# Kernel optimization log

Measured on AMD Instinct MI355X. Metric: run time of the kernel, lower is better.

The kernel has to match this reference:

```python
import jax, jax.numpy as jnp
import numpy as np


def _next_pow2(n: int) -> int:
    return 1 << (int(n) - 1).bit_length()


def setup_inputs() -> dict:
    key = jax.random.key(0)
    k1, k2 = jax.random.split(key)
    B, T, L = 256, 65536, 65536  # batch, seq_len, filter length (L >= T so epoched recurrence == full causal conv)
    x = jax.random.normal(k1, (B, T), dtype=jnp.float32)
    filt = jax.random.normal(k2, (1, L), dtype=jnp.float32) / np.float32(np.sqrt(L))
    return {"x": x, "filt": filt}


def reference(x, filt):
    """EpochedFutureFill.forward == causal FIR convolution of x with filt.

    The torch module's per-token loop (sliced dot-product + FFT-refreshed
    FutureFill cache every K steps) computes exactly
        y[:, t] = sum_{s=0}^{t} filt[0, s] * x[:, t - s]
    for t < T <= L. We express that directly as one FFT convolution,
    mirroring the module's own future_fill (pow-2 rfft/irfft) math.
    """
    B, T = x.shape
    L = filt.shape[-1]
    n_fft = _next_pow2(T + L - 1)
    xf = jnp.fft.rfft(x, n=n_fft)        # (B, n_fft//2+1) complex
    ff = jnp.fft.rfft(filt, n=n_fft)     # (1, n_fft//2+1) complex, broadcasts over batch
    y_full = jnp.fft.irfft(xf * ff, n=n_fft)
    return y_full[:, :T]                 # causal part: (B, T)
```

## Files before the change

kernel.cpp:

```cpp
#include <hip/hip_runtime.h>


#define N_FFT 131072
#define N1    512
#define N2    256
#define T_LEN 65536
#define CB    128
#define PI_F  3.14159265358979323846f
#define R2_F  0.70710678118654752f

__device__ inline int brev9(int x) { return (int)(__brev((unsigned)x) >> 23); }

__device__ inline float2 cadd(float2 a, float2 b){ return make_float2(a.x+b.x, a.y+b.y); }
__device__ inline float2 csub(float2 a, float2 b){ return make_float2(a.x-b.x, a.y-b.y); }
__device__ inline float2 cmul(float2 a, float2 b){ return make_float2(a.x*b.x-a.y*b.y, a.x*b.y+a.y*b.x); }
__device__ inline float2 expif(float a){ float s,c; __sincosf(a,&s,&c); return make_float2(c,s); }

__device__ inline void dif4(float2&a0, float2&a1, float2&a2, float2&a3, float2 w1, float2 w2){
    float2 s02 = cadd(a0,a2), d02 = csub(a0,a2);
    float2 s13 = cadd(a1,a3), d13 = csub(a1,a3);
    float2 b2 = cmul(w1,d02);
    float2 t  = cmul(w1,d13);
    float2 b3 = make_float2(t.y, -t.x);
    a0 = cadd(s02,s13);
    a1 = cmul(w2, csub(s02,s13));
    a2 = cadd(b2,b3);
    a3 = cmul(w2, csub(b2,b3));
}

__device__ inline void dit4i(float2&a0, float2&a1, float2&a2, float2&a3, float2 w1, float2 w2){
    float2 t1 = cmul(w1,a1), t3 = cmul(w1,a3);
    float2 u0 = cadd(a0,t1), u1 = csub(a0,t1);
    float2 u2 = cadd(a2,t3), u3 = csub(a2,t3);
    float2 s2 = cmul(w2,u2), s3 = cmul(w2,u3);
    a0 = cadd(u0,s2); a2 = csub(u0,s2);
    a1 = make_float2(u1.x - s3.y, u1.y + s3.x);
    a3 = make_float2(u1.x + s3.y, u1.y - s3.x);
}

__global__ __launch_bounds__(512, 4) void fwd_cols(
    const float* __restrict__ re_base, const float* __restrict__ im_base,
    long long row_stride, float2* __restrict__ dst)
{
    __shared__ float2 s[N1 * 16];
    const int tile = blockIdx.x, row = blockIdx.y, tid = threadIdx.x;
    const int n2base = tile * 16;
    const float* rp = re_base + (long long)row * row_stride;
    const float* ip = im_base ? (im_base + (long long)row * row_stride) : nullptr;

    {
        const int cp = tid & 7, n1g = tid >> 3;
#pragma unroll
        for (int i = 0; i < 4; i++) {
            int n1 = n1g + 64 * i;
            int g  = n1 * N2 + n2base + 2 * cp;
            float2 a = *(const float2*)(rp + g);
            float2 b = ip ? *(const float2*)(ip + g) : make_float2(0.f, 0.f);
            s[n1 * 16 + 2 * cp]     = make_float2(a.x, b.x);
            s[n1 * 16 + 2 * cp + 1] = make_float2(a.y, b.y);
        }
    }
    __syncthreads();

    const int c = tid & 15, r = tid >> 4;

#pragma unroll
    for (int qq = 0; qq < 4; qq++) {
        int j = r + 32 * qq;
        float2 w1 = expif((float)j * (-PI_F / 256.f));
        float2 w2 = cmul(w1, w1);
        float2 a0 = s[j * 16 + c], a1 = s[(j + 128) * 16 + c];
        float2 b2 = cmul(w1, a0);
        float2 t  = cmul(w1, a1);
        float2 b3 = make_float2(t.y, -t.x);
        s[j * 16 + c]         = cadd(a0, a1);
        s[(j + 128) * 16 + c] = cmul(w2, csub(a0, a1));
        s[(j + 256) * 16 + c] = cadd(b2, b3);
        s[(j + 384) * 16 + c] = cmul(w2, csub(b2, b3));
    }
    __syncthreads();

#pragma unroll
    for (int qq = 0; qq < 4; qq++) {
        int q = r + 32 * qq, j = q & 31, g = q >> 5;
        int p0 = g * 128 + j;
        float2 w1 = expif((float)j * (-PI_F / 64.f));
        float2 w2 = cmul(w1, w1);
        float2 a0 = s[p0*16+c], a1 = s[(p0+32)*16+c], a2 = s[(p0+64)*16+c], a3 = s[(p0+96)*16+c];
        dif4(a0, a1, a2, a3, w1, w2);
        s[p0*16+c] = a0; s[(p0+32)*16+c] = a1; s[(p0+64)*16+c] = a2; s[(p0+96)*16+c] = a3;
    }
    __syncthreads();

#pragma unroll
    for (int qq = 0; qq < 4; qq++) {
        int q = r + 32 * qq, j = q & 7, g = q >> 3;
        int p0 = g * 32 + j;
        float2 w1 = expif((float)j * (-PI_F / 16.f));
        float2 w2 = cmul(w1, w1);
        float2 a0 = s[p0*16+c], a1 = s[(p0+8)*16+c], a2 = s[(p0+16)*16+c], a3 = s[(p0+24)*16+c];
        dif4(a0, a1, a2, a3, w1, w2);
        s[p0*16+c] = a0; s[(p0+8)*16+c] = a1; s[(p0+16)*16+c] = a2; s[(p0+24)*16+c] = a3;
    }
    __syncthreads();

    float2* drow = dst + (size_t)row * N_FFT;
    const int n2 = n2base + c;
    const float2 w1c = make_float2(R2_F, -R2_F);
    const float2 w2c = make_float2(0.f, -1.f);
    const float2 one = make_float2(1.f, 0.f);
#pragma unroll
    for (int o = 0; o < 2; o++) {
        int base = 8 * (r + 32 * o);
        float2 v[8];
#pragma unroll
        for (int m = 0; m < 8; m++) v[m] = s[(base + m) * 16 + c];
        dif4(v[0], v[2], v[4], v[6], one, one);
        dif4(v[1], v[3], v[5], v[7], w1c, w2c);
#pragma unroll
        for (int m = 0; m < 8; m += 2) {
            float2 a = v[m], b = v[m + 1];
            v[m] = cadd(a, b); v[m + 1] = csub(a, b);
        }
#pragma unroll
        for (int m = 0; m < 8; m++) {
            int p  = base + m;
            int k1 = brev9(p);
            float2 w = expif((float)(n2 * k1) * (-2.f * PI_F / (float)N_FFT));
            drow[(size_t)k1 * N2 + n2] = cmul(v[m], w);
        }
    }
}

#define MROW 292
#define MIDX(rw, p) ((rw) * MROW + (p) + ((p) >> 3))

__global__ __launch_bounds__(256) void fwd_rows_g(float2* __restrict__ G)
{
    __shared__ float2 s[8 * MROW];
    const int tid = threadIdx.x;
    const long long rbase = (long long)blockIdx.x * 8;
#pragma unroll
    for (int i = 0; i < 8; i++) {
        int e = tid + 256 * i, rw = e >> 8, p = e & 255;
        s[MIDX(rw, p)] = G[(rbase + rw) * N2 + p];
    }
    __syncthreads();
    const int rl = tid >> 5, rr = tid & 31;
#pragma unroll
    for (int qq = 0; qq < 2; qq++) {
        int j = rr + 32 * qq;
        float2 w1 = expif((float)j * (-PI_F / 128.f)), w2 = cmul(w1, w1);
        float2 a0=s[MIDX(rl,j)], a1=s[MIDX(rl,j+64)], a2=s[MIDX(rl,j+128)], a3=s[MIDX(rl,j+192)];
        dif4(a0,a1,a2,a3,w1,w2);
        s[MIDX(rl,j)]=a0; s[MIDX(rl,j+64)]=a1; s[MIDX(rl,j+128)]=a2; s[MIDX(rl,j+192)]=a3;
    }
    __syncthreads();
#pragma unroll
    for (int qq = 0; qq < 2; qq++) {
        int q = rr + 32 * qq, j = q & 15, g = q >> 4, p0 = g * 64 + j;
        float2 w1 = expif((float)j * (-PI_F / 32.f)), w2 = cmul(w1, w1);
        float2 a0=s[MIDX(rl,p0)], a1=s[MIDX(rl,p0+16)], a2=s[MIDX(rl,p0+32)], a3=s[MIDX(rl,p0+48)];
        dif4(a0,a1,a2,a3,w1,w2);
        s[MIDX(rl,p0)]=a0; s[MIDX(rl,p0+16)]=a1; s[MIDX(rl,p0+32)]=a2; s[MIDX(rl,p0+48)]=a3;
    }
    __syncthreads();
#pragma unroll
    for (int qq = 0; qq < 2; qq++) {
        int q = rr + 32 * qq, j = q & 3, g = q >> 2, p0 = g * 16 + j;
        float2 w1 = expif((float)j * (-PI_F / 8.f)), w2 = cmul(w1, w1);
        float2 a0=s[MIDX(rl,p0)], a1=s[MIDX(rl,p0+4)], a2=s[MIDX(rl,p0+8)], a3=s[MIDX(rl,p0+12)];
        dif4(a0,a1,a2,a3,w1,w2);
        s[MIDX(rl,p0)]=a0; s[MIDX(rl,p0+4)]=a1; s[MIDX(rl,p0+8)]=a2; s[MIDX(rl,p0+12)]=a3;
    }
    __syncthreads();
#pragma unroll
    for (int qq = 0; qq < 2; qq++) {
        int base = 4 * (rr + 32 * qq);
        float2 a0=s[MIDX(rl,base)], a1=s[MIDX(rl,base+1)], a2=s[MIDX(rl,base+2)], a3=s[MIDX(rl,base+3)];
        float2 s02 = cadd(a0,a2), d02 = csub(a0,a2);
        float2 s13 = cadd(a1,a3), d13 = csub(a1,a3);
        float2 b3 = make_float2(d13.y, -d13.x);
        s[MIDX(rl,base)]   = cadd(s02,s13);
        s[MIDX(rl,base+1)] = csub(s02,s13);
        s[MIDX(rl,base+2)] = cadd(d02,b3);
        s[MIDX(rl,base+3)] = csub(d02,b3);
    }
    __syncthreads();
#pragma unroll
    for (int i = 0; i < 8; i++) {
        int e = tid + 256 * i, rw = e >> 8, p = e & 255;
        G[(rbase + rw) * N2 + p] = s[MIDX(rw, p)];
    }
}

__global__ __launch_bounds__(256) void mid_rows(
    float2* __restrict__ buf, const float2* __restrict__ Gb)
{
    __shared__ float2 s[8 * MROW];
    const int tid = threadIdx.x;
    const long long rbase = (long long)blockIdx.x * 8;
#pragma unroll
    for (int i = 0; i < 8; i++) {
        int e = tid + 256 * i, rw = e >> 8, p = e & 255;
        s[MIDX(rw, p)] = buf[(rbase + rw) * N2 + p];
    }
    __syncthreads();
    const int rl = tid >> 5, rr = tid & 31;
    const int k1 = (int)((rbase + rl) & (N1 - 1));

#pragma unroll
    for (int qq = 0; qq < 2; qq++) {
        int j = rr + 32 * qq;
        float2 w1 = expif((float)j * (-PI_F / 128.f)), w2 = cmul(w1, w1);
        float2 a0=s[MIDX(rl,j)], a1=s[MIDX(rl,j+64)], a2=s[MIDX(rl,j+128)], a3=s[MIDX(rl,j+192)];
        dif4(a0,a1,a2,a3,w1,w2);
        s[MIDX(rl,j)]=a0; s[MIDX(rl,j+64)]=a1; s[MIDX(rl,j+128)]=a2; s[MIDX(rl,j+192)]=a3;
    }
    __syncthreads();
#pragma unroll
    for (int qq = 0; qq < 2; qq++) {
        int q = rr + 32 * qq, j = q & 15, g = q >> 4, p0 = g * 64 + j;
        float2 w1 = expif((float)j * (-PI_F / 32.f)), w2 = cmul(w1, w1);
        float2 a0=s[MIDX(rl,p0)], a1=s[MIDX(rl,p0+16)], a2=s[MIDX(rl,p0+32)], a3=s[MIDX(rl,p0+48)];
        dif4(a0,a1,a2,a3,w1,w2);
        s[MIDX(rl,p0)]=a0; s[MIDX(rl,p0+16)]=a1; s[MIDX(rl,p0+32)]=a2; s[MIDX(rl,p0+48)]=a3;
    }
    __syncthreads();
#pragma unroll
    for (int qq = 0; qq < 2; qq++) {
        int q = rr + 32 * qq, j = q & 3, g = q >> 2, p0 = g * 16 + j;
        float2 w1 = expif((float)j * (-PI_F / 8.f)), w2 = cmul(w1, w1);
        float2 a0=s[MIDX(rl,p0)], a1=s[MIDX(rl,p0+4)], a2=s[MIDX(rl,p0+8)], a3=s[MIDX(rl,p0+12)];
        dif4(a0,a1,a2,a3,w1,w2);
        s[MIDX(rl,p0)]=a0; s[MIDX(rl,p0+4)]=a1; s[MIDX(rl,p0+8)]=a2; s[MIDX(rl,p0+12)]=a3;
    }
    __syncthreads();

    const float2* grow = Gb + (size_t)k1 * N2;
#pragma unroll
    for (int qq = 0; qq < 2; qq++) {
        int base = 4 * (rr + 32 * qq);
        float2 a0=s[MIDX(rl,base)], a1=s[MIDX(rl,base+1)], a2=s[MIDX(rl,base+2)], a3=s[MIDX(rl,base+3)];
        float2 s02 = cadd(a0,a2), d02 = csub(a0,a2);
        float2 s13 = cadd(a1,a3), d13 = csub(a1,a3);
        float2 b3 = make_float2(d13.y, -d13.x);
        float2 v0 = cadd(s02,s13), v1 = csub(s02,s13), v2 = cadd(d02,b3), v3 = csub(d02,b3);
        v0 = cmul(v0, grow[base]);   v1 = cmul(v1, grow[base+1]);
        v2 = cmul(v2, grow[base+2]); v3 = cmul(v3, grow[base+3]);
        float2 u0 = cadd(v0,v1), u1 = csub(v0,v1);
        float2 u2 = cadd(v2,v3), u3 = csub(v2,v3);
        s[MIDX(rl,base)]   = cadd(u0,u2);
        s[MIDX(rl,base+2)] = csub(u0,u2);
        s[MIDX(rl,base+1)] = make_float2(u1.x - u3.y, u1.y + u3.x);
        s[MIDX(rl,base+3)] = make_float2(u1.x + u3.y, u1.y - u3.x);
    }
    __syncthreads();

#pragma unroll
    for (int qq = 0; qq < 2; qq++) {
        int q = rr + 32 * qq, j = q & 3, g = q >> 2, p0 = g * 16 + j;
        float2 w2 = expif((float)j * (PI_F / 8.f)), w1 = cmul(w2, w2);
        float2 a0=s[MIDX(rl,p0)], a1=s[MIDX(rl,p0+4)], a2=s[MIDX(rl,p0+8)], a3=s[MIDX(rl,p0+12)];
        dit4i(a0,a1,a2,a3,w1,w2);
        s[MIDX(rl,p0)]=a0; s[MIDX(rl,p0+4)]=a1; s[MIDX(rl,p0+8)]=a2; s[MIDX(rl,p0+12)]=a3;
    }
    __syncthreads();
#pragma unroll
    for (int qq = 0; qq < 2; qq++) {
        int q = rr + 32 * qq, j = q & 15, g = q >> 4, p0 = g * 64 + j;
        float2 w2 = expif((float)j * (PI_F / 32.f)), w1 = cmul(w2, w2);
        float2 a0=s[MIDX(rl,p0)], a1=s[MIDX(rl,p0+16)], a2=s[MIDX(rl,p0+32)], a3=s[MIDX(rl,p0+48)];
        dit4i(a0,a1,a2,a3,w1,w2);
        s[MIDX(rl,p0)]=a0; s[MIDX(rl,p0+16)]=a1; s[MIDX(rl,p0+32)]=a2; s[MIDX(rl,p0+48)]=a3;
    }
    __syncthreads();
#pragma unroll
    for (int qq = 0; qq < 2; qq++) {
        int j = rr + 32 * qq;
        float2 w2 = expif((float)j * (PI_F / 128.f)), w1 = cmul(w2, w2);
        float2 a0=s[MIDX(rl,j)], a1=s[MIDX(rl,j+64)], a2=s[MIDX(rl,j+128)], a3=s[MIDX(rl,j+192)];
        dit4i(a0,a1,a2,a3,w1,w2);
        s[MIDX(rl,j)]=a0; s[MIDX(rl,j+64)]=a1; s[MIDX(rl,j+128)]=a2; s[MIDX(rl,j+192)]=a3;
    }
    __syncthreads();

#pragma unroll
    for (int i = 0; i < 8; i++) {
        int e = tid + 256 * i, rw = e >> 8, p = e & 255;
        int kk = (int)((rbase + rw) & (N1 - 1));
        float2 w = expif((float)(p * kk) * (2.f * PI_F / (float)N_FFT));
        buf[(rbase + rw) * N2 + p] = cmul(s[MIDX(rw, p)], w);
    }
}

__global__ __launch_bounds__(512, 4) void inv_cols(
    const float2* __restrict__ src, float* __restrict__ out)
{
    __shared__ float2 s[N1 * 16];
    const int tile = blockIdx.x, row = blockIdx.y, tid = threadIdx.x;
    const int n2base = tile * 16;
    const int c = tid & 15, r = tid >> 4;
    const float2* srow = src + (size_t)row * N_FFT;

#pragma unroll
    for (int i = 0; i < 16; i++) {
        int k1 = r + 32 * i;
        s[brev9(k1) * 16 + c] = srow[(size_t)k1 * N2 + n2base + c];
    }
    __syncthreads();

    const float2 w1c = make_float2(0.f, 1.f);
    const float2 w2c = make_float2(R2_F, R2_F);
    const float2 one = make_float2(1.f, 0.f);
#pragma unroll
    for (int o = 0; o < 2; o++) {
        int base = 8 * (r + 32 * o);
        float2 v[8];
#pragma unroll
        for (int m = 0; m < 8; m++) v[m] = s[(base + m) * 16 + c];
#pragma unroll
        for (int m = 0; m < 8; m += 2) {
            float2 a = v[m], b = v[m + 1];
            v[m] = cadd(a, b); v[m + 1] = csub(a, b);
        }
        dit4i(v[0], v[2], v[4], v[6], one, one);
        dit4i(v[1], v[3], v[5], v[7], w1c, w2c);
#pragma unroll
        for (int m = 0; m < 8; m++) s[(base + m) * 16 + c] = v[m];
    }
    __syncthreads();

#pragma unroll
    for (int qq = 0; qq < 4; qq++) {
        int q = r + 32 * qq, j = q & 7, g = q >> 3, p0 = g * 32 + j;
        float2 w2 = expif((float)j * (PI_F / 16.f)), w1 = cmul(w2, w2);
        float2 a0 = s[p0*16+c], a1 = s[(p0+8)*16+c], a2 = s[(p0+16)*16+c], a3 = s[(p0+24)*16+c];
        dit4i(a0, a1, a2, a3, w1, w2);
        s[p0*16+c] = a0; s[(p0+8)*16+c] = a1; s[(p0+16)*16+c] = a2; s[(p0+24)*16+c] = a3;
    }
    __syncthreads();
#pragma unroll
    for (int qq = 0; qq < 4; qq++) {
        int q = r + 32 * qq, j = q & 31, g = q >> 5, p0 = g * 128 + j;
        float2 w2 = expif((float)j * (PI_F / 64.f)), w1 = cmul(w2, w2);
        float2 a0 = s[p0*16+c], a1 = s[(p0+32)*16+c], a2 = s[(p0+64)*16+c], a3 = s[(p0+96)*16+c];
        dit4i(a0, a1, a2, a3, w1, w2);
        s[p0*16+c] = a0; s[(p0+32)*16+c] = a1; s[(p0+64)*16+c] = a2; s[(p0+96)*16+c] = a3;
    }
    __syncthreads();
#pragma unroll
    for (int qq = 0; qq < 4; qq++) {
        int j = r + 32 * qq;
        float2 w2 = expif((float)j * (PI_F / 256.f)), w1 = cmul(w2, w2);
        float2 a0 = s[j*16+c], a1 = s[(j+128)*16+c], a2 = s[(j+256)*16+c], a3 = s[(j+384)*16+c];
        dit4i(a0, a1, a2, a3, w1, w2);
        s[j*16+c] = a0; s[(j+128)*16+c] = a1; s[(j+256)*16+c] = a2; s[(j+384)*16+c] = a3;
    }
    __syncthreads();

    const float scale = 1.0f / (float)N_FFT;
    float* out0 = out + (size_t)(2 * row) * T_LEN;
    float* out1 = out + (size_t)(2 * row + 1) * T_LEN;
#pragma unroll
    for (int i = 0; i < 8; i++) {
        int p = r + 32 * i;
        int n = p * N2 + n2base + c;
        float2 v = s[p * 16 + c];
        out0[n] = v.x * scale;
        out1[n] = v.y * scale;
    }
}

extern "C" void kernel_launch(void* const* d_in, const int* in_sizes, int n_in,
                              void* d_out, int out_size, void* d_ws, size_t ws_size,
                              hipStream_t stream) {
    const float* x    = (const float*)d_in[0];
    const float* filt = (const float*)d_in[1];
    float* out = (float*)d_out;

    float2* buf = (float2*)d_ws;
    float2* G   = (float2*)((char*)d_ws + (size_t)CB * N_FFT * sizeof(float2));

    fwd_cols<<<dim3(16, 1), 512, 0, stream>>>(filt, nullptr, 0LL, G);
    fwd_rows_g<<<N1 / 8, 256, 0, stream>>>(G);
    fwd_cols<<<dim3(16, CB), 512, 0, stream>>>(x, x + T_LEN, (long long)(2 * T_LEN), buf);
    mid_rows<<<(CB * N1) / 8, 256, 0, stream>>>(buf, G);
    inv_cols<<<dim3(16, CB), 512, 0, stream>>>(buf, out);
}
```

Measured before the change: 254.3 us.

## Store intermediate FFT buffer in fp16 and vectorize mid/inv kernels

The large intermediate spectrum buffer between the column and row FFT passes is now stored as packed fp16 instead of float2, halving global traffic across three kernels. mid_rows moves to 512 threads with float4 shared-memory accesses and a new padding layout, and inv_cols loads and stores vectorized. fwd_cols computes output twiddles by recurrence instead of one sincos per element. The fp16 intermediate lowers accuracy and could break tolerance for long convolutions.

```diff
diff --git a/kernel.cpp b/kernel.cpp
--- a/kernel.cpp
+++ b/kernel.cpp
@@ -9,12 +9,16 @@
 #define PI_F  3.14159265358979323846f
 #define R2_F  0.70710678118654752f
 
+typedef __attribute__((ext_vector_type(2))) __fp16 h2;
+typedef __attribute__((ext_vector_type(4))) __fp16 h4;
+
 __device__ inline int brev9(int x) { return (int)(__brev((unsigned)x) >> 23); }
 
 __device__ inline float2 cadd(float2 a, float2 b){ return make_float2(a.x+b.x, a.y+b.y); }
 __device__ inline float2 csub(float2 a, float2 b){ return make_float2(a.x-b.x, a.y-b.y); }
 __device__ inline float2 cmul(float2 a, float2 b){ return make_float2(a.x*b.x-a.y*b.y, a.x*b.y+a.y*b.x); }
 __device__ inline float2 expif(float a){ float s,c; __sincosf(a,&s,&c); return make_float2(c,s); }
+__device__ inline h2 f2h(float2 v){ return __builtin_amdgcn_cvt_pkrtz(v.x, v.y); }
 
 __device__ inline void dif4(float2&a0, float2&a1, float2&a2, float2&a3, float2 w1, float2 w2){
     float2 s02 = cadd(a0,a2), d02 = csub(a0,a2);
@@ -38,9 +42,10 @@
     a3 = make_float2(u1.x + s3.y, u1.y - s3.x);
 }
 
+template<bool HALF>
 __global__ __launch_bounds__(512, 4) void fwd_cols(
     const float* __restrict__ re_base, const float* __restrict__ im_base,
-    long long row_stride, float2* __restrict__ dst)
+    long long row_stride, void* __restrict__ dstv)
 {
     __shared__ float2 s[N1 * 16];
     const int tile = blockIdx.x, row = blockIdx.y, tid = threadIdx.x;
@@ -104,11 +109,11 @@
     }
     __syncthreads();
 
-    float2* drow = dst + (size_t)row * N_FFT;
     const int n2 = n2base + c;
     const float2 w1c = make_float2(R2_F, -R2_F);
     const float2 w2c = make_float2(0.f, -1.f);
     const float2 one = make_float2(1.f, 0.f);
+    const float2 w64 = expif((float)n2 * (-PI_F / 1024.f));
 #pragma unroll
     for (int o = 0; o < 2; o++) {
         int base = 8 * (r + 32 * o);
@@ -122,18 +127,32 @@
             float2 a = v[m], b = v[m + 1];
             v[m] = cadd(a, b); v[m + 1] = csub(a, b);
         }
+        const int Kb = brev9(base);
+        float2 wK = expif((float)(n2 * Kb) * (-2.f * PI_F / (float)N_FFT));
+        float2 pw[8];
+        pw[0] = one;
+#pragma unroll
+        for (int k = 1; k < 8; k++) pw[k] = cmul(pw[k-1], w64);
+        const int b3tab[8] = {0,4,2,6,1,5,3,7};
 #pragma unroll
         for (int m = 0; m < 8; m++) {
-            int p  = base + m;
-            int k1 = brev9(p);
-            float2 w = expif((float)(n2 * k1) * (-2.f * PI_F / (float)N_FFT));
-            drow[(size_t)k1 * N2 + n2] = cmul(v[m], w);
+            int b  = b3tab[m];
+            int k1 = Kb + 64 * b;
+            float2 w = cmul(wK, pw[b]);
+            float2 rv = cmul(v[m], w);
+            if (HALF) {
+                h2* drow = (h2*)dstv + (size_t)row * N_FFT;
+                drow[(size_t)k1 * N2 + n2] = f2h(rv);
+            } else {
+                float2* drow = (float2*)dstv + (size_t)row * N_FFT;
+                drow[(size_t)k1 * N2 + n2] = rv;
+            }
         }
     }
 }
 
-#define MROW 292
-#define MIDX(rw, p) ((rw) * MROW + (p) + ((p) >> 3))
+#define MROW 288
+#define MIDX(rw, p) ((rw) * MROW + (p) + 2 * ((p) >> 4))
 
 __global__ __launch_bounds__(256) void fwd_rows_g(float2* __restrict__ G)
 {
@@ -194,42 +213,44 @@
     }
 }
 
-__global__ __launch_bounds__(256) void mid_rows(
-    float2* __restrict__ buf, const float2* __restrict__ Gb)
+__global__ __launch_bounds__(512) void mid_rows(
+    h2* __restrict__ buf, const float2* __restrict__ Gb)
 {
-    __shared__ float2 s[8 * MROW];
+    __shared__ float4 s4[(8 * MROW) / 2];
+    float2* s = (float2*)s4;
     const int tid = threadIdx.x;
     const long long rbase = (long long)blockIdx.x * 8;
-#pragma unroll
-    for (int i = 0; i < 8; i++) {
-        int e = tid + 256 * i, rw = e >> 8, p = e & 255;
-        s[MIDX(rw, p)] = buf[(rbase + rw) * N2 + p];
-    }
-    __syncthreads();
-    const int rl = tid >> 5, rr = tid & 31;
+
+#pragma unroll
+    for (int i = 0; i < 2; i++) {
+        int e = tid + 512 * i;
+        int rw = e >> 7, pp = (e & 127) * 2;
+        h4 v = *((const h4*)(buf + (rbase + rw) * N2 + pp));
+        s4[MIDX(rw, pp) >> 1] = make_float4((float)v.x, (float)v.y, (float)v.z, (float)v.w);
+    }
+    __syncthreads();
+
+    const int rl = tid >> 6, rr = tid & 63;
     const int k1 = (int)((rbase + rl) & (N1 - 1));
 
-#pragma unroll
-    for (int qq = 0; qq < 2; qq++) {
-        int j = rr + 32 * qq;
+    {
+        int j = rr;
         float2 w1 = expif((float)j * (-PI_F / 128.f)), w2 = cmul(w1, w1);
         float2 a0=s[MIDX(rl,j)], a1=s[MIDX(rl,j+64)], a2=s[MIDX(rl,j+128)], a3=s[MIDX(rl,j+192)];
         dif4(a0,a1,a2,a3,w1,w2);
         s[MIDX(rl,j)]=a0; s[MIDX(rl,j+64)]=a1; s[MIDX(rl,j+128)]=a2; s[MIDX(rl,j+192)]=a3;
     }
     __syncthreads();
-#pragma unroll
-    for (int qq = 0; qq < 2; qq++) {
-        int q = rr + 32 * qq, j = q & 15, g = q >> 4, p0 = g * 64 + j;
+    {
+        int j = rr & 15, g = rr >> 4, p0 = g * 64 + j;
         float2 w1 = expif((float)j * (-PI_F / 32.f)), w2 = cmul(w1, w1);
         float2 a0=s[MIDX(rl,p0)], a1=s[MIDX(rl,p0+16)], a2=s[MIDX(rl,p0+32)], a3=s[MIDX(rl,p0+48)];
         dif4(a0,a1,a2,a3,w1,w2);
         s[MIDX(rl,p0)]=a0; s[MIDX(rl,p0+16)]=a1; s[MIDX(rl,p0+32)]=a2; s[MIDX(rl,p0+48)]=a3;
     }
     __syncthreads();
-#pragma unroll
-    for (int qq = 0; qq < 2; qq++) {
-        int q = rr + 32 * qq, j = q & 3, g = q >> 2, p0 = g * 16 + j;
+    {
+        int j = rr & 3, g = rr >> 2, p0 = g * 16 + j;
         float2 w1 = expif((float)j * (-PI_F / 8.f)), w2 = cmul(w1, w1);
         float2 a0=s[MIDX(rl,p0)], a1=s[MIDX(rl,p0+4)], a2=s[MIDX(rl,p0+8)], a3=s[MIDX(rl,p0+12)];
         dif4(a0,a1,a2,a3,w1,w2);
@@ -237,47 +258,50 @@
     }
     __syncthreads();
 
-    const float2* grow = Gb + (size_t)k1 * N2;
-#pragma unroll
-    for (int qq = 0; qq < 2; qq++) {
-        int base = 4 * (rr + 32 * qq);
-        float2 a0=s[MIDX(rl,base)], a1=s[MIDX(rl,base+1)], a2=s[MIDX(rl,base+2)], a3=s[MIDX(rl,base+3)];
+    {
+        int base = 4 * rr;
+        int si = MIDX(rl, base) >> 1;
+        float4 q01 = s4[si], q23 = s4[si + 1];
+        float2 a0 = make_float2(q01.x, q01.y), a1 = make_float2(q01.z, q01.w);
+        float2 a2 = make_float2(q23.x, q23.y), a3 = make_float2(q23.z, q23.w);
         float2 s02 = cadd(a0,a2), d02 = csub(a0,a2);
         float2 s13 = cadd(a1,a3), d13 = csub(a1,a3);
         float2 b3 = make_float2(d13.y, -d13.x);
         float2 v0 = cadd(s02,s13), v1 = csub(s02,s13), v2 = cadd(d02,b3), v3 = csub(d02,b3);
-        v0 = cmul(v0, grow[base]);   v1 = cmul(v1, grow[base+1]);
-        v2 = cmul(v2, grow[base+2]); v3 = cmul(v3, grow[base+3]);
+        const float4* g4 = (const float4*)(Gb + (size_t)k1 * N2);
+        float4 g01 = g4[base >> 1], g23 = g4[(base >> 1) + 1];
+        v0 = cmul(v0, make_float2(g01.x, g01.y));
+        v1 = cmul(v1, make_float2(g01.z, g01.w));
+        v2 = cmul(v2, make_float2(g23.x, g23.y));
+        v3 = cmul(v3, make_float2(g23.z, g23.w));
         float2 u0 = cadd(v0,v1), u1 = csub(v0,v1);
         float2 u2 = cadd(v2,v3), u3 = csub(v2,v3);
-        s[MIDX(rl,base)]   = cadd(u0,u2);
-        s[MIDX(rl,base+2)] = csub(u0,u2);
-        s[MIDX(rl,base+1)] = make_float2(u1.x - u3.y, u1.y + u3.x);
-        s[MIDX(rl,base+3)] = make_float2(u1.x + u3.y, u1.y - u3.x);
-    }
-    __syncthreads();
-
-#pragma unroll
-    for (int qq = 0; qq < 2; qq++) {
-        int q = rr + 32 * qq, j = q & 3, g = q >> 2, p0 = g * 16 + j;
+        float2 r0 = cadd(u0,u2), r2 = csub(u0,u2);
+        float2 r1 = make_float2(u1.x - u3.y, u1.y + u3.x);
+        float2 r3 = make_float2(u1.x + u3.y, u1.y - u3.x);
+        s4[si]     = make_float4(r0.x, r0.y, r1.x, r1.y);
+        s4[si + 1] = make_float4(r2.x, r2.y, r3.x, r3.y);
+    }
+    __syncthreads();
+
+    {
+        int j = rr & 3, g = rr >> 2, p0 = g * 16 + j;
         float2 w2 = expif((float)j * (PI_F / 8.f)), w1 = cmul(w2, w2);
         float2 a0=s[MIDX(rl,p0)], a1=s[MIDX(rl,p0+4)], a2=s[MIDX(rl,p0+8)], a3=s[MIDX(rl,p0+12)];
         dit4i(a0,a1,a2,a3,w1,w2);
         s[MIDX(rl,p0)]=a0; s[MIDX(rl,p0+4)]=a1; s[MIDX(rl,p0+8)]=a2; s[MIDX(rl,p0+12)]=a3;
     }
     __syncthreads();
-#pragma unroll
-    for (int qq = 0; qq < 2; qq++) {
-        int q = rr + 32 * qq, j = q & 15, g = q >> 4, p0 = g * 64 + j;
+    {
+        int j = rr & 15, g = rr >> 4, p0 = g * 64 + j;
         float2 w2 = expif((float)j * (PI_F / 32.f)), w1 = cmul(w2, w2);
         float2 a0=s[MIDX(rl,p0)], a1=s[MIDX(rl,p0+16)], a2=s[MIDX(rl,p0+32)], a3=s[MIDX(rl,p0+48)];
         dit4i(a0,a1,a2,a3,w1,w2);
         s[MIDX(rl,p0)]=a0; s[MIDX(rl,p0+16)]=a1; s[MIDX(rl,p0+32)]=a2; s[MIDX(rl,p0+48)]=a3;
     }
     __syncthreads();
-#pragma unroll
-    for (int qq = 0; qq < 2; qq++) {
-        int j = rr + 32 * qq;
+    {
+        int j = rr;
         float2 w2 = expif((float)j * (PI_F / 128.f)), w1 = cmul(w2, w2);
         float2 a0=s[MIDX(rl,j)], a1=s[MIDX(rl,j+64)], a2=s[MIDX(rl,j+128)], a3=s[MIDX(rl,j+192)];
         dit4i(a0,a1,a2,a3,w1,w2);
@@ -286,29 +310,41 @@
     __syncthreads();
 
 #pragma unroll
-    for (int i = 0; i < 8; i++) {
-        int e = tid + 256 * i, rw = e >> 8, p = e & 255;
+    for (int i = 0; i < 2; i++) {
+        int e = tid + 512 * i;
+        int rw = e >> 7, pp = (e & 127) * 2;
         int kk = (int)((rbase + rw) & (N1 - 1));
-        float2 w = expif((float)(p * kk) * (2.f * PI_F / (float)N_FFT));
-        buf[(rbase + rw) * N2 + p] = cmul(s[MIDX(rw, p)], w);
+        float4 q = s4[MIDX(rw, pp) >> 1];
+        float2 wA = expif((float)(pp * kk) * (2.f * PI_F / (float)N_FFT));
+        float2 wB = expif((float)((pp + 1) * kk) * (2.f * PI_F / (float)N_FFT));
+        float2 rA = cmul(make_float2(q.x, q.y), wA);
+        float2 rB = cmul(make_float2(q.z, q.w), wB);
+        h2 ha = f2h(rA), hb = f2h(rB);
+        h4 o; o.x = ha.x; o.y = ha.y; o.z = hb.x; o.w = hb.y;
+        *((h4*)(buf + (rbase + rw) * N2 + pp)) = o;
     }
 }
 
 __global__ __launch_bounds__(512, 4) void inv_cols(
-    const float2* __restrict__ src, float* __restrict__ out)
+    const h2* __restrict__ src, float* __restrict__ out)
 {
-    __shared__ float2 s[N1 * 16];
+    __shared__ float4 s4[N1 * 16 / 2];
+    float2* s = (float2*)s4;
     const int tile = blockIdx.x, row = blockIdx.y, tid = threadIdx.x;
     const int n2base = tile * 16;
+    const h2* srow = src + (size_t)row * N_FFT;
+    const int cp = tid & 7, r8 = tid >> 3;
+
+#pragma unroll
+    for (int i = 0; i < 8; i++) {
+        int k1 = r8 + 64 * i;
+        h4 v = *((const h4*)(srow + (size_t)k1 * N2 + n2base + 2 * cp));
+        int p = brev9(k1);
+        s4[p * 8 + cp] = make_float4((float)v.x, (float)v.y, (float)v.z, (float)v.w);
+    }
+    __syncthreads();
+
     const int c = tid & 15, r = tid >> 4;
-    const float2* srow = src + (size_t)row * N_FFT;
-
-#pragma unroll
-    for (int i = 0; i < 16; i++) {
-        int k1 = r + 32 * i;
-        s[brev9(k1) * 16 + c] = srow[(size_t)k1 * N2 + n2base + c];
-    }
-    __syncthreads();
 
     const float2 w1c = make_float2(0.f, 1.f);
     const float2 w2c = make_float2(R2_F, R2_F);
@@ -363,12 +399,12 @@
     float* out0 = out + (size_t)(2 * row) * T_LEN;
     float* out1 = out + (size_t)(2 * row + 1) * T_LEN;
 #pragma unroll
-    for (int i = 0; i < 8; i++) {
-        int p = r + 32 * i;
-        int n = p * N2 + n2base + c;
-        float2 v = s[p * 16 + c];
-        out0[n] = v.x * scale;
-        out1[n] = v.y * scale;
+    for (int i = 0; i < 4; i++) {
+        int p = r8 + 64 * i;
+        float4 q = s4[p * 8 + cp];
+        int n = p * N2 + n2base + 2 * cp;
+        *(float2*)(out0 + n) = make_float2(q.x * scale, q.z * scale);
+        *(float2*)(out1 + n) = make_float2(q.y * scale, q.w * scale);
     }
 }
 
@@ -379,12 +415,12 @@
     const float* filt = (const float*)d_in[1];
     float* out = (float*)d_out;
 
-    float2* buf = (float2*)d_ws;
-    float2* G   = (float2*)((char*)d_ws + (size_t)CB * N_FFT * sizeof(float2));
-
-    fwd_cols<<<dim3(16, 1), 512, 0, stream>>>(filt, nullptr, 0LL, G);
+    h2* buf = (h2*)d_ws;
+    float2* G = (float2*)((char*)d_ws + (size_t)CB * N_FFT * sizeof(h2));
+
+    fwd_cols<false><<<dim3(16, 1), 512, 0, stream>>>(filt, nullptr, 0LL, (void*)G);
     fwd_rows_g<<<N1 / 8, 256, 0, stream>>>(G);
-    fwd_cols<<<dim3(16, CB), 512, 0, stream>>>(x, x + T_LEN, (long long)(2 * T_LEN), buf);
-    mid_rows<<<(CB * N1) / 8, 256, 0, stream>>>(buf, G);
+    fwd_cols<true><<<dim3(16, CB), 512, 0, stream>>>(x, x + T_LEN, (long long)(2 * T_LEN), (void*)buf);
+    mid_rows<<<(CB * N1) / 8, 512, 0, stream>>>(buf, G);
     inv_cols<<<dim3(16, CB), 512, 0, stream>>>(buf, out);
 }
```

After: 234.2 us. 7.9% less time.
